# Optimization experiments

Hardware: AMD Instinct MI355X
Metric: run time of the kernel (lower is better)

The kernel has to match this reference:

```python
import jax, jax.numpy as jnp
import numpy as np

VIEWS = 32   # hardcoded in forward
K = 5        # LocalGCN k
D = 1024     # (34-2)*(34-2) flattened conv features per view
EPS = 1e-5   # BatchNorm eps


def leaky_relu(x, slope=0.2):
    return jnp.where(x >= 0, x, slope * x)


def setup_inputs() -> dict:
    key = jax.random.key(0)
    ks = jax.random.split(key, 8)
    B_img = 512 * VIEWS
    x = jax.random.normal(ks[0], (B_img, 3, 34, 34), jnp.float32)
    vertices = jax.random.normal(ks[1], (VIEWS, 3), jnp.float32)
    # Conv2d(3, 1, 3)
    conv_w = jax.random.normal(ks[2], (1, 3, 3, 3), jnp.float32) * 0.1
    conv_b = jnp.zeros((1,), jnp.float32)
    # relation MLP R: Linear(10,10) -> ReLU -> Linear(10,1)
    r_w1 = jax.random.normal(ks[3], (10, 10), jnp.float32) * 0.3
    r_b1 = jnp.zeros((10,), jnp.float32)
    r_w2 = jax.random.normal(ks[4], (1, 10), jnp.float32) * 0.3
    r_b2 = jnp.zeros((1,), jnp.float32)
    # LocalGCN conv: Linear(D, D) + BatchNorm1d(D)
    lin_w = jax.random.normal(ks[5], (D, D), jnp.float32) / np.sqrt(D)
    lin_b = jnp.zeros((D,), jnp.float32)
    bn_g = jnp.ones((D,), jnp.float32)
    bn_b = jnp.zeros((D,), jnp.float32)
    return dict(x=x, vertices=vertices, conv_w=conv_w, conv_b=conv_b,
                r_w1=r_w1, r_b1=r_b1, r_w2=r_w2, r_b2=r_b2,
                lin_w=lin_w, lin_b=lin_b, bn_g=bn_g, bn_b=bn_b)


def reference(x, vertices, conv_w, conv_b, r_w1, r_b1, r_w2, r_b2,
              lin_w, lin_b, bn_g, bn_b):
    # Conv2d(3->1, kernel 3, valid) : (B*32,3,34,34) -> (B*32,1,32,32)
    y = jax.lax.conv_general_dilated(
        x, conv_w, window_strides=(1, 1), padding='VALID',
        dimension_numbers=('NCHW', 'OIHW', 'NCHW'))
    y = y + conv_b[None, :, None, None]

    B = x.shape[0] // VIEWS
    F = y.reshape(B, VIEWS, D)                       # (B, N, D)
    V = jnp.broadcast_to(vertices[None], (B, VIEWS, 3))  # (B, N, 3)

    # knn over vertices: negative squared pairwise distance, topk largest
    inner = -2.0 * jnp.einsum('bnd,bmd->bnm', V, V)
    xx = jnp.sum(V * V, axis=-1, keepdims=True)
    pdist = -xx - inner - jnp.swapaxes(xx, 1, 2)     # (B, N, N)
    idx = jax.lax.top_k(pdist, K)[1]                 # (B, N, K)

    # index_points gathers
    Fn = jax.vmap(lambda p, i: p[i])(F, idx)         # (B, N, K, D)
    Vn = jax.vmap(lambda p, i: p[i])(V, idx)         # (B, N, K, 3)

    v0 = jnp.broadcast_to(Vn[:, :, :1, :], Vn.shape)
    dv = v0 - Vn
    dnorm = jnp.sqrt(jnp.sum(dv * dv, axis=-1, keepdims=True) + 1e-12)
    v_F = jnp.concatenate([v0, Vn, dv, dnorm], axis=-1)   # (B, N, K, 10)

    h = jax.nn.relu(v_F @ r_w1.T + r_b1)
    e = h @ r_w2.T + r_b2                            # (B, N, K, 1)

    Fa = jnp.sum(e * Fn, axis=2)                     # (B, N, D)

    flat = Fa.reshape(-1, D)
    z = flat @ lin_w.T + lin_b
    mean = jnp.mean(z, axis=0)
    var = jnp.var(z, axis=0)
    z = (z - mean) / jnp.sqrt(var + EPS) * bn_g + bn_b
    out = leaky_relu(z).reshape(-1, 1, D)            # n_views = 1
    return out
```

## Files before the change

### kernel.cpp

```cpp
#include <hip/hip_runtime.h>
#include <stdint.h>

typedef unsigned short u16;
using bf16x8 = __attribute__((ext_vector_type(8))) short;
using f32x4  = __attribute__((ext_vector_type(4))) float;

__device__ __forceinline__ float bf2f(u16 u) {
  union { unsigned int i; float f; } a; a.i = ((unsigned int)u) << 16; return a.f;
}
__device__ __forceinline__ u16 f2bf(float f) {
  union { float f; unsigned int i; } a; a.f = f;
  unsigned int u = a.i;
  u += 0x7fffu + ((u >> 16) & 1u);
  return (u16)(u >> 16);
}
__device__ __forceinline__ float lrelu(float x) { return x >= 0.f ? x : 0.2f * x; }

__global__ __launch_bounds__(256) void prep_convw_kernel(
    const float* __restrict__ vert, const float* __restrict__ rw1,
    const float* __restrict__ rb1, const float* __restrict__ rw2,
    const float* __restrict__ rb2, const float* __restrict__ lw,
    u16* __restrict__ wb, float* __restrict__ e_out,
    int* __restrict__ idx_out, float* __restrict__ stats) {
  const int t = threadIdx.x;
  if (blockIdx.x < 1024) {
    const int i = blockIdx.x * 256 + t;
    float4 v = ((const float4*)lw)[i];
    uint2 o;
    o.x = (unsigned)f2bf(v.x) | ((unsigned)f2bf(v.y) << 16);
    o.y = (unsigned)f2bf(v.z) | ((unsigned)f2bf(v.w) << 16);
    ((uint2*)wb)[i] = o;
    return;
  }
  __shared__ float Vs[96];
  __shared__ float w1s[100];
  __shared__ float b1s[10];
  __shared__ float w2s[10];
  __shared__ float b2s;
  if (t < 96)  Vs[t]  = vert[t];
  if (t < 100) w1s[t] = rw1[t];
  if (t < 10)  { b1s[t] = rb1[t]; w2s[t] = rw2[t]; }
  if (t == 0)  b2s = rb2[0];
  for (int i = t; i < 2048; i += 256) stats[i] = 0.f;
  __syncthreads();
  if (t < 32) {
    const float vt0 = Vs[t*3], vt1 = Vs[t*3+1], vt2 = Vs[t*3+2];
    const float xxt = vt0*vt0 + vt1*vt1 + vt2*vt2;
    float pd[32];
    #pragma unroll
    for (int m = 0; m < 32; ++m) {
      float m0 = Vs[m*3], m1 = Vs[m*3+1], m2 = Vs[m*3+2];
      float dot = vt0*m0 + vt1*m1 + vt2*m2;
      float inner = -2.f * dot;
      float xxm = m0*m0 + m1*m1 + m2*m2;
      pd[m] = -xxt - inner - xxm;
    }
    int sel[5];
    unsigned taken = 0;
    #pragma unroll
    for (int k = 0; k < 5; ++k) {
      float best = -3.0e38f; int bi = 0;
      #pragma unroll
      for (int m = 0; m < 32; ++m)
        if (!((taken >> m) & 1u) && pd[m] > best) { best = pd[m]; bi = m; }
      taken |= (1u << bi);
      sel[k] = bi;
    }
    const int s0 = sel[0];
    const float v0x = Vs[s0*3], v0y = Vs[s0*3+1], v0z = Vs[s0*3+2];
    #pragma unroll
    for (int k = 0; k < 5; ++k) {
      const int si = sel[k];
      float vx = Vs[si*3], vy = Vs[si*3+1], vz = Vs[si*3+2];
      float dx = v0x - vx, dy = v0y - vy, dz = v0z - vz;
      float dn = sqrtf(dx*dx + dy*dy + dz*dz + 1e-12f);
      float vF[10] = {v0x, v0y, v0z, vx, vy, vz, dx, dy, dz, dn};
      float e = b2s;
      #pragma unroll
      for (int i = 0; i < 10; ++i) {
        float h = b1s[i];
        #pragma unroll
        for (int j = 0; j < 10; ++j) h += w1s[i*10+j] * vF[j];
        h = h > 0.f ? h : 0.f;
        e += w2s[i] * h;
      }
      e_out[t*5+k]   = e;
      idx_out[t*5+k] = sel[k];
    }
  }
}

__global__ __launch_bounds__(256) void conv_gather_kernel(
    const float* __restrict__ x, const float* __restrict__ cw,
    const float* __restrict__ cb, const float* __restrict__ e,
    const int* __restrict__ idx, u16* __restrict__ Fa) {
  __shared__ __align__(16) float img[3*34*34];
  __shared__ __align__(16) u16 Fl[32*1024];
  __shared__ float e_s[160];
  __shared__ int   idx_s[160];
  const int t = threadIdx.x;
  const long b = blockIdx.x;

  float w[27];
  #pragma unroll
  for (int q = 0; q < 27; ++q) w[q] = cw[q];
  const float bias = cb[0];
  if (t < 160) { e_s[t] = e[t]; idx_s[t] = idx[t]; }

  const int p0 = t * 4;
  const int i = p0 >> 5, j = p0 & 31;
  for (int v = 0; v < 32; ++v) {
    const float4* src = (const float4*)(x + (b*32 + v) * 3468);
    for (int q = t; q < 867; q += 256)
      ((float4*)img)[q] = src[q];
    __syncthreads();
    u16 r[4];
    #pragma unroll
    for (int u = 0; u < 4; ++u) {
      float acc = bias;
      #pragma unroll
      for (int c = 0; c < 3; ++c)
        #pragma unroll
        for (int dy = 0; dy < 3; ++dy)
          #pragma unroll
          for (int dxk = 0; dxk < 3; ++dxk)
            acc += w[c*9 + dy*3 + dxk] * img[c*1156 + (i+dy)*34 + (j+u+dxk)];
      r[u] = f2bf(acc);
    }
    uint2 o;
    o.x = (unsigned)r[0] | ((unsigned)r[1] << 16);
    o.y = (unsigned)r[2] | ((unsigned)r[3] << 16);
    ((uint2*)(Fl + v*1024))[t] = o;
    __syncthreads();
  }
  for (int n = 0; n < 32; ++n) {
    float a0=0.f, a1=0.f, a2=0.f, a3=0.f;
    #pragma unroll
    for (int k = 0; k < 5; ++k) {
      const float ek = e_s[n*5+k];
      const int id = idx_s[n*5+k];
      uint2 d = ((const uint2*)(Fl + id*1024))[t];
      a0 += ek * __uint_as_float(d.x << 16);
      a1 += ek * __uint_as_float(d.x & 0xffff0000u);
      a2 += ek * __uint_as_float(d.y << 16);
      a3 += ek * __uint_as_float(d.y & 0xffff0000u);
    }
    uint2 o;
    o.x = (unsigned)f2bf(a0) | ((unsigned)f2bf(a1) << 16);
    o.y = (unsigned)f2bf(a2) | ((unsigned)f2bf(a3) << 16);
    ((uint2*)(Fa + (b*32 + n) * 1024))[t] = o;
  }
}

__global__ __launch_bounds__(256) void gemm_kernel(const u16* __restrict__ A,
    const u16* __restrict__ W, const float* __restrict__ linb, u16* __restrict__ z,
    float* __restrict__ stats) {
  __shared__ __align__(16) u16 At[128*32];
  __shared__ __align__(16) u16 Bt[128*32];
  const int t = threadIdx.x;
  const int lane = t & 63;
  const int w = t >> 6;
  const int lr = lane & 15, lq = lane >> 4;
  const int wm = w >> 1, wn = w & 1;
  const long m0 = (long)blockIdx.y * 128;
  const int n0 = blockIdx.x * 128;
  f32x4 acc[4][4];
  #pragma unroll
  for (int mi = 0; mi < 4; ++mi)
    #pragma unroll
    for (int ni = 0; ni < 4; ++ni) acc[mi][ni] = (f32x4){0.f, 0.f, 0.f, 0.f};
  const int srow = t >> 2;
  const int scol = (t & 3) * 8;
  for (int k0 = 0; k0 < 1024; k0 += 32) {
    #pragma unroll
    for (int h = 0; h < 2; ++h) {
      const u16* ga = A + (m0 + h*64 + srow) * 1024 + k0 + scol;
      const u16* gb = W + (long)(n0 + h*64 + srow) * 1024 + k0 + scol;
      __builtin_amdgcn_global_load_lds(
          (const __attribute__((address_space(1))) void*)ga,
          (__attribute__((address_space(3))) void*)((char*)At + h*4096 + t*16), 16, 0, 0);
      __builtin_amdgcn_global_load_lds(
          (const __attribute__((address_space(1))) void*)gb,
          (__attribute__((address_space(3))) void*)((char*)Bt + h*4096 + t*16), 16, 0, 0);
    }
    __syncthreads();
    bf16x8 af[4], bfr[4];
    #pragma unroll
    for (int i = 0; i < 4; ++i)
      af[i] = *(const bf16x8*)&At[(wm*64 + i*16 + lr)*32 + lq*8];
    #pragma unroll
    for (int i = 0; i < 4; ++i)
      bfr[i] = *(const bf16x8*)&Bt[(wn*64 + i*16 + lr)*32 + lq*8];
    #pragma unroll
    for (int mi = 0; mi < 4; ++mi)
      #pragma unroll
      for (int ni = 0; ni < 4; ++ni)
        acc[mi][ni] = __builtin_amdgcn_mfma_f32_16x16x32_bf16(af[mi], bfr[ni], acc[mi][ni], 0, 0, 0);
    __syncthreads();
  }
  #pragma unroll
  for (int ni = 0; ni < 4; ++ni) {
    const int col = n0 + wn*64 + ni*16 + lr;
    const float bias = linb[col];
    float s = 0.f, q = 0.f;
    #pragma unroll
    for (int mi = 0; mi < 4; ++mi) {
      const long row = m0 + wm*64 + mi*16 + lq*4;
      #pragma unroll
      for (int r = 0; r < 4; ++r) {
        const float v = acc[mi][ni][r] + bias;
        z[(row + r) * 1024 + col] = f2bf(v);
        s += v; q += v * v;
      }
    }
    s += __shfl_xor(s, 16); q += __shfl_xor(q, 16);
    s += __shfl_xor(s, 32); q += __shfl_xor(q, 32);
    if (lq == 0) {
      atomicAdd(&stats[col], s);
      atomicAdd(&stats[1024 + col], q);
    }
  }
}

__global__ __launch_bounds__(256) void norm_kernel(const u16* __restrict__ z,
    const float* __restrict__ stats, const float* __restrict__ g,
    const float* __restrict__ bb, float invM, float* __restrict__ out) {
  const int t = threadIdx.x;
  const long i = (long)blockIdx.x * 256 + t;
  uint4 d = ((const uint4*)z)[i];
  const int c = (t & 127) * 8;
  float vv[8];
  vv[0] = __uint_as_float(d.x << 16); vv[1] = __uint_as_float(d.x & 0xffff0000u);
  vv[2] = __uint_as_float(d.y << 16); vv[3] = __uint_as_float(d.y & 0xffff0000u);
  vv[4] = __uint_as_float(d.z << 16); vv[5] = __uint_as_float(d.z & 0xffff0000u);
  vv[6] = __uint_as_float(d.w << 16); vv[7] = __uint_as_float(d.w & 0xffff0000u);
  float y[8];
  #pragma unroll
  for (int j = 0; j < 8; ++j) {
    const int cj = c + j;
    const float mean = stats[cj] * invM;
    const float var  = stats[1024+cj] * invM - mean*mean;
    const float sc = g[cj] * rsqrtf(var + 1e-5f);
    const float sh = bb[cj] - mean * sc;
    y[j] = lrelu(vv[j] * sc + sh);
  }
  float4 o0 = {y[0], y[1], y[2], y[3]};
  float4 o1 = {y[4], y[5], y[6], y[7]};
  ((float4*)out)[i*2]   = o0;
  ((float4*)out)[i*2+1] = o1;
}

extern "C" void kernel_launch(void* const* d_in, const int* in_sizes, int n_in,
                              void* d_out, int out_size, void* d_ws, size_t ws_size,
                              hipStream_t stream) {
  const float* x    = (const float*)d_in[0];
  const float* vert = (const float*)d_in[1];
  const float* cw   = (const float*)d_in[2];
  const float* cb   = (const float*)d_in[3];
  const float* rw1  = (const float*)d_in[4];
  const float* rb1  = (const float*)d_in[5];
  const float* rw2  = (const float*)d_in[6];
  const float* rb2  = (const float*)d_in[7];
  const float* lw   = (const float*)d_in[8];
  const float* lb   = (const float*)d_in[9];
  const float* bng  = (const float*)d_in[10];
  const float* bnb  = (const float*)d_in[11];
  float* out = (float*)d_out;

  const int n_img = in_sizes[0] / (3*34*34);
  const size_t faBytes = (size_t)n_img * 1024 * 2;

  char* ws = (char*)d_ws;
  u16*  Fa = (u16*)ws;
  u16*  z  = (u16*)(ws + faBytes);
  char* sp = ws + 2*faBytes;
  float* e_buf   = (float*)sp;
  int*   idx_buf = (int*)(sp + 1024);
  float* stats   = (float*)(sp + 2048);
  u16*   Wb      = (u16*)(sp + 16384);

  prep_convw_kernel<<<1025, 256, 0, stream>>>(vert, rw1, rb1, rw2, rb2, lw, Wb,
                                              e_buf, idx_buf, stats);
  conv_gather_kernel<<<n_img/32, 256, 0, stream>>>(x, cw, cb, e_buf, idx_buf, Fa);
  gemm_kernel<<<dim3(8, n_img/128), 256, 0, stream>>>(Fa, Wb, lb, z, stats);
  norm_kernel<<<n_img/2, 256, 0, stream>>>(z, stats, bng, bnb, 1.f/(float)n_img, out);
}
```

Before: 475.3 us.

## Split fused conv+gather into per-image conv and per-view gather kernels

Replaces the fused conv/gather kernel, which ran one block per batch of 32 views with a serial per-view loop and about 80KB of LDS, with two kernels. One computes each image's convolution in its own block, and the other performs the K-neighbor weighted gather from a global bf16 intermediate. This gives far more blocks and lower LDS use per block, so occupancy and latency hiding should improve. The cost is an extra launch and a 32MB global round trip for F, which reuses the z buffer region.

```diff
diff --git a/kernel.cpp b/kernel.cpp
--- a/kernel.cpp
+++ b/kernel.cpp
@@ -90,66 +90,60 @@
   }
 }
 
-__global__ __launch_bounds__(256) void conv_gather_kernel(
-    const float* __restrict__ x, const float* __restrict__ cw,
-    const float* __restrict__ cb, const float* __restrict__ e,
-    const int* __restrict__ idx, u16* __restrict__ Fa) {
-  __shared__ __align__(16) float img[3*34*34];
-  __shared__ __align__(16) u16 Fl[32*1024];
-  __shared__ float e_s[160];
-  __shared__ int   idx_s[160];
-  const int t = threadIdx.x;
-  const long b = blockIdx.x;
-
+__global__ __launch_bounds__(256) void conv_kernel(const float* __restrict__ x,
+    const float* __restrict__ cw, const float* __restrict__ cb, u16* __restrict__ F) {
+  __shared__ __align__(16) float lds[3*34*34];
+  const int t = threadIdx.x;
+  const long img = blockIdx.x;
+  const float4* src = (const float4*)(x + img * 3468);
+  for (int q = t; q < 867; q += 256)
+    ((float4*)lds)[q] = src[q];
   float w[27];
   #pragma unroll
   for (int q = 0; q < 27; ++q) w[q] = cw[q];
   const float bias = cb[0];
-  if (t < 160) { e_s[t] = e[t]; idx_s[t] = idx[t]; }
-
+  __syncthreads();
   const int p0 = t * 4;
   const int i = p0 >> 5, j = p0 & 31;
-  for (int v = 0; v < 32; ++v) {
-    const float4* src = (const float4*)(x + (b*32 + v) * 3468);
-    for (int q = t; q < 867; q += 256)
-      ((float4*)img)[q] = src[q];
-    __syncthreads();
-    u16 r[4];
-    #pragma unroll
-    for (int u = 0; u < 4; ++u) {
-      float acc = bias;
-      #pragma unroll
-      for (int c = 0; c < 3; ++c)
+  u16 r[4];
+  #pragma unroll
+  for (int u = 0; u < 4; ++u) {
+    float acc = bias;
+    #pragma unroll
+    for (int c = 0; c < 3; ++c)
+      #pragma unroll
+      for (int dy = 0; dy < 3; ++dy)
         #pragma unroll
-        for (int dy = 0; dy < 3; ++dy)
-          #pragma unroll
-          for (int dxk = 0; dxk < 3; ++dxk)
-            acc += w[c*9 + dy*3 + dxk] * img[c*1156 + (i+dy)*34 + (j+u+dxk)];
-      r[u] = f2bf(acc);
-    }
-    uint2 o;
-    o.x = (unsigned)r[0] | ((unsigned)r[1] << 16);
-    o.y = (unsigned)r[2] | ((unsigned)r[3] << 16);
-    ((uint2*)(Fl + v*1024))[t] = o;
-    __syncthreads();
-  }
-  for (int n = 0; n < 32; ++n) {
-    float a0=0.f, a1=0.f, a2=0.f, a3=0.f;
-    #pragma unroll
-    for (int k = 0; k < 5; ++k) {
-      const float ek = e_s[n*5+k];
-      const int id = idx_s[n*5+k];
-      uint2 d = ((const uint2*)(Fl + id*1024))[t];
-      a0 += ek * __uint_as_float(d.x << 16);
-      a1 += ek * __uint_as_float(d.x & 0xffff0000u);
-      a2 += ek * __uint_as_float(d.y << 16);
-      a3 += ek * __uint_as_float(d.y & 0xffff0000u);
-    }
-    uint2 o;
-    o.x = (unsigned)f2bf(a0) | ((unsigned)f2bf(a1) << 16);
-    o.y = (unsigned)f2bf(a2) | ((unsigned)f2bf(a3) << 16);
-    ((uint2*)(Fa + (b*32 + n) * 1024))[t] = o;
-  }
+        for (int dxk = 0; dxk < 3; ++dxk)
+          acc += w[c*9 + dy*3 + dxk] * lds[c*1156 + (i+dy)*34 + (j+u+dxk)];
+    r[u] = f2bf(acc);
+  }
+  uint2 o;
+  o.x = (unsigned)r[0] | ((unsigned)r[1] << 16);
+  o.y = (unsigned)r[2] | ((unsigned)r[3] << 16);
+  ((uint2*)(F + img*1024))[t] = o;
+}
+
+__global__ __launch_bounds__(256) void gather_kernel(const u16* __restrict__ F,
+    const float* __restrict__ e, const int* __restrict__ idx, u16* __restrict__ Fa) {
+  const int g = blockIdx.x;
+  const int b = g >> 5, n = g & 31;
+  const int t = threadIdx.x;
+  float a0=0.f, a1=0.f, a2=0.f, a3=0.f;
+  #pragma unroll
+  for (int k = 0; k < 5; ++k) {
+    const float ek = e[n*5+k];
+    const int id = idx[n*5+k];
+    uint2 d = ((const uint2*)(F + ((long)(b*32 + id)) * 1024))[t];
+    a0 += ek * __uint_as_float(d.x << 16);
+    a1 += ek * __uint_as_float(d.x & 0xffff0000u);
+    a2 += ek * __uint_as_float(d.y << 16);
+    a3 += ek * __uint_as_float(d.y & 0xffff0000u);
+  }
+  uint2 o;
+  o.x = (unsigned)f2bf(a0) | ((unsigned)f2bf(a1) << 16);
+  o.y = (unsigned)f2bf(a2) | ((unsigned)f2bf(a3) << 16);
+  ((uint2*)(Fa + (long)g * 1024))[t] = o;
 }
 
 __global__ __launch_bounds__(256) void gemm_kernel(const u16* __restrict__ A,
@@ -272,6 +266,7 @@
 
   char* ws = (char*)d_ws;
   u16*  Fa = (u16*)ws;
+  u16*  F  = (u16*)(ws + faBytes);
   u16*  z  = (u16*)(ws + faBytes);
   char* sp = ws + 2*faBytes;
   float* e_buf   = (float*)sp;
@@ -281,7 +276,8 @@
 
   prep_convw_kernel<<<1025, 256, 0, stream>>>(vert, rw1, rb1, rw2, rb2, lw, Wb,
                                               e_buf, idx_buf, stats);
-  conv_gather_kernel<<<n_img/32, 256, 0, stream>>>(x, cw, cb, e_buf, idx_buf, Fa);
+  conv_kernel<<<n_img, 256, 0, stream>>>(x, cw, cb, F);
+  gather_kernel<<<n_img, 256, 0, stream>>>(F, e_buf, idx_buf, Fa);
   gemm_kernel<<<dim3(8, n_img/128), 256, 0, stream>>>(Fa, Wb, lb, z, stats);
   norm_kernel<<<n_img/2, 256, 0, stream>>>(z, stats, bng, bnb, 1.f/(float)n_img, out);
 }
```

Result: faster. 461.9 us (-2.8%).
